# Kernel optimization log

Hardware: AMD Instinct MI355X
Metric: run time of the kernel (lower is better)

Reference implementation:

```python
import jax, jax.numpy as jnp
import numpy as np

TAU_M = 5.0 / 3.0
V_TH = 1.0


def setup_inputs() -> dict:
    key = jax.random.key(0)
    T, B, C, H, W = 8, 32, 128, 32, 32
    x = jax.random.normal(key, (T, B, C, H, W), dtype=jnp.float32)
    return {"x": x}


def reference(x):
    """LIF neuron: leaky integrate, bidirectional threshold fire (+1/-1), hard reset.
    x: [T, B, C, H, W]. Returns spike train output: [T, B, C, H, W]."""
    def step(V, x_t):
        dv = -V / TAU_M + x_t          # leak + input current
        V_new = V + dv                  # integrate
        out = (V_new >= V_TH).astype(x_t.dtype) - (V_new <= -V_TH).astype(x_t.dtype)
        V_next = (1.0 - jnp.abs(out)) * V_new   # reset to 0 where spiked
        return V_next, out

    V0 = jnp.zeros_like(x[0])
    _, output = jax.lax.scan(step, V0, x)
    return output
```

## Files before the change

kernel.cpp:

```cpp
#include <hip/hip_runtime.h>


#define T_STEPS 8

typedef float vfloat4 __attribute__((ext_vector_type(4)));

struct StepOut { float V; float o; };

__device__ __forceinline__ StepOut lif_step(float V, float x) {
    const float TAU = (float)(5.0 / 3.0);
    float dv = (-V) / TAU + x;
    float Vn = V + dv;
    float o = (Vn >= 1.0f ? 1.0f : 0.0f) - (Vn <= -1.0f ? 1.0f : 0.0f);
    StepOut r;
    r.o = o;
    r.V = (o == 0.0f) ? Vn : 0.0f;
    return r;
}

__device__ __forceinline__ vfloat4 lif_step4(vfloat4& V, vfloat4 xt) {
    StepOut a = lif_step(V.x, xt.x);
    StepOut b = lif_step(V.y, xt.y);
    StepOut c = lif_step(V.z, xt.z);
    StepOut d = lif_step(V.w, xt.w);
    vfloat4 Vn, o;
    Vn.x = a.V; Vn.y = b.V; Vn.z = c.V; Vn.w = d.V;
    o.x = a.o;  o.y = b.o;  o.z = c.o;  o.w = d.o;
    V = Vn;
    return o;
}

__global__ __launch_bounds__(256) void lif_kernel(const vfloat4* __restrict__ x,
                                                  vfloat4* __restrict__ out,
                                                  int n4) {
    const int Q = n4 >> 2;
    int q = blockIdx.x * blockDim.x + threadIdx.x;
    if (q >= Q) return;

    const size_t s = (size_t)n4;
    const size_t i0 = (size_t)q;
    const size_t i1 = (size_t)q + (size_t)Q;
    const size_t i2 = (size_t)q + 2 * (size_t)Q;
    const size_t i3 = (size_t)q + 3 * (size_t)Q;

    vfloat4 Va = (vfloat4)(0.f);
    vfloat4 Vb = Va, Vc = Va, Vd = Va;

#pragma unroll
    for (int t = 0; t < T_STEPS; ++t) {
        const size_t base = (size_t)t * s;
        vfloat4 xa = x[base + i0];
        vfloat4 xb = x[base + i1];
        vfloat4 xc = x[base + i2];
        vfloat4 xd = x[base + i3];

        vfloat4 oa = lif_step4(Va, xa);
        vfloat4 ob = lif_step4(Vb, xb);
        vfloat4 oc = lif_step4(Vc, xc);
        vfloat4 od = lif_step4(Vd, xd);

        __builtin_nontemporal_store(oa, &out[base + i0]);
        __builtin_nontemporal_store(ob, &out[base + i1]);
        __builtin_nontemporal_store(oc, &out[base + i2]);
        __builtin_nontemporal_store(od, &out[base + i3]);
    }
}

extern "C" void kernel_launch(void* const* d_in, const int* in_sizes, int n_in,
                              void* d_out, int out_size, void* d_ws, size_t ws_size,
                              hipStream_t stream) {
    const float* x = (const float*)d_in[0];
    float* out = (float*)d_out;

    int total = in_sizes[0];
    int n = total / T_STEPS;
    int n4 = n / 4;
    int Q = n4 / 4;

    dim3 block(256);
    dim3 grid((Q + block.x - 1) / block.x);
    lif_kernel<<<grid, block, 0, stream>>>((const vfloat4*)x, (vfloat4*)out, n4);
}
```

Baseline: 232.0 us.

## Issue all timestep loads up front via inline asm, one vec4 per thread

Each thread now handles a single float4 column instead of four. All eight timestep loads are issued back to back through inline-asm global_load_dwordx4, followed by one explicit vmcnt(0) wait, so that every read is in flight before any compute starts. The grid grows 4x to keep enough parallelism, and stores switch from nontemporal to ordinary stores. The risks are that the hand-written asm and explicit wait limit the compiler's own scheduling, and that dropping nontemporal stores may pollute the cache.

```diff
diff --git a/kernel.cpp b/kernel.cpp
--- a/kernel.cpp
+++ b/kernel.cpp
@@ -30,40 +30,44 @@
     return o;
 }
 
-__global__ __launch_bounds__(256) void lif_kernel(const vfloat4* __restrict__ x,
-                                                  vfloat4* __restrict__ out,
+#define ASM_LOAD(dst, addr)                                        \
+    asm volatile("global_load_dwordx4 %0, %1, off"                 \
+                 : "=&v"(dst)                                      \
+                 : "v"(addr))
+
+__global__ __launch_bounds__(256) void lif_kernel(const float* __restrict__ x,
+                                                  float* __restrict__ out,
                                                   int n4) {
-    const int Q = n4 >> 2;
-    int q = blockIdx.x * blockDim.x + threadIdx.x;
-    if (q >= Q) return;
+    int i = blockIdx.x * blockDim.x + threadIdx.x;
+    if (i >= n4) return;
+
+    const unsigned long long stride = (unsigned long long)n4 * 16ull;
+    unsigned long long a = (unsigned long long)x + (unsigned long long)i * 16ull;
+
+    vfloat4 x0, x1, x2, x3, x4, x5, x6, x7;
+    ASM_LOAD(x0, a + 0 * stride);
+    ASM_LOAD(x1, a + 1 * stride);
+    ASM_LOAD(x2, a + 2 * stride);
+    ASM_LOAD(x3, a + 3 * stride);
+    ASM_LOAD(x4, a + 4 * stride);
+    ASM_LOAD(x5, a + 5 * stride);
+    ASM_LOAD(x6, a + 6 * stride);
+    ASM_LOAD(x7, a + 7 * stride);
+    asm volatile("s_waitcnt vmcnt(0)"
+                 : "+v"(x0), "+v"(x1), "+v"(x2), "+v"(x3),
+                   "+v"(x4), "+v"(x5), "+v"(x6), "+v"(x7));
 
     const size_t s = (size_t)n4;
-    const size_t i0 = (size_t)q;
-    const size_t i1 = (size_t)q + (size_t)Q;
-    const size_t i2 = (size_t)q + 2 * (size_t)Q;
-    const size_t i3 = (size_t)q + 3 * (size_t)Q;
-
-    vfloat4 Va = (vfloat4)(0.f);
-    vfloat4 Vb = Va, Vc = Va, Vd = Va;
-
-#pragma unroll
-    for (int t = 0; t < T_STEPS; ++t) {
-        const size_t base = (size_t)t * s;
-        vfloat4 xa = x[base + i0];
-        vfloat4 xb = x[base + i1];
-        vfloat4 xc = x[base + i2];
-        vfloat4 xd = x[base + i3];
-
-        vfloat4 oa = lif_step4(Va, xa);
-        vfloat4 ob = lif_step4(Vb, xb);
-        vfloat4 oc = lif_step4(Vc, xc);
-        vfloat4 od = lif_step4(Vd, xd);
-
-        __builtin_nontemporal_store(oa, &out[base + i0]);
-        __builtin_nontemporal_store(ob, &out[base + i1]);
-        __builtin_nontemporal_store(oc, &out[base + i2]);
-        __builtin_nontemporal_store(od, &out[base + i3]);
-    }
+    vfloat4* o4 = (vfloat4*)out;
+    vfloat4 V = (vfloat4)(0.f);
+    o4[0 * s + i] = lif_step4(V, x0);
+    o4[1 * s + i] = lif_step4(V, x1);
+    o4[2 * s + i] = lif_step4(V, x2);
+    o4[3 * s + i] = lif_step4(V, x3);
+    o4[4 * s + i] = lif_step4(V, x4);
+    o4[5 * s + i] = lif_step4(V, x5);
+    o4[6 * s + i] = lif_step4(V, x6);
+    o4[7 * s + i] = lif_step4(V, x7);
 }
 
 extern "C" void kernel_launch(void* const* d_in, const int* in_sizes, int n_in,
@@ -75,9 +79,8 @@
     int total = in_sizes[0];
     int n = total / T_STEPS;
     int n4 = n / 4;
-    int Q = n4 / 4;
 
     dim3 block(256);
-    dim3 grid((Q + block.x - 1) / block.x);
-    lif_kernel<<<grid, block, 0, stream>>>((const vfloat4*)x, (vfloat4*)out, n4);
+    dim3 grid((n4 + block.x - 1) / block.x);
+    lif_kernel<<<grid, block, 0, stream>>>(x, out, n4);
 }
```

Result: slower. 239.6 us (+3.2%).

## Split LIF into pack kernel with 2-bit spike codes and unpack kernel

Applied to the files above, without the earlier changes.

Splits the fused LIF kernel into two launches. The first loads all 8 timesteps at once with inline-asm loads and a single wait, computes the spikes and packs them as 2-bit codes into a 64-bit workspace word per float4 lane. The second reads those words and writes the decoded float outputs. The intent is to separate the read-heavy and write-heavy phases so each streams more efficiently, at the cost of an extra launch and a small workspace round trip.

```diff
diff --git a/kernel.cpp b/kernel.cpp
--- a/kernel.cpp
+++ b/kernel.cpp
@@ -18,6 +18,77 @@
     return r;
 }
 
+__device__ __forceinline__ unsigned enc(float o) {
+    return (o == 1.0f) ? 1u : ((o == -1.0f) ? 2u : 0u);
+}
+
+__device__ __forceinline__ float dec(unsigned c) {
+    return (c == 1u) ? 1.0f : ((c == 2u) ? -1.0f : 0.0f);
+}
+
+#define ASM_LOAD(dst, addr)                                        \
+    asm volatile("global_load_dwordx4 %0, %1, off"                 \
+                 : "=&v"(dst)                                      \
+                 : "v"(addr))
+
+__global__ __launch_bounds__(256) void lif_pack(const float* __restrict__ x,
+                                                unsigned long long* __restrict__ ws,
+                                                int n4) {
+    int i = blockIdx.x * blockDim.x + threadIdx.x;
+    if (i >= n4) return;
+
+    const unsigned long long stride = (unsigned long long)n4 * 16ull;
+    unsigned long long a = (unsigned long long)x + (unsigned long long)i * 16ull;
+
+    vfloat4 x0, x1, x2, x3, x4, x5, x6, x7;
+    ASM_LOAD(x0, a + 0 * stride);
+    ASM_LOAD(x1, a + 1 * stride);
+    ASM_LOAD(x2, a + 2 * stride);
+    ASM_LOAD(x3, a + 3 * stride);
+    ASM_LOAD(x4, a + 4 * stride);
+    ASM_LOAD(x5, a + 5 * stride);
+    ASM_LOAD(x6, a + 6 * stride);
+    ASM_LOAD(x7, a + 7 * stride);
+    asm volatile("s_waitcnt vmcnt(0)"
+                 : "+v"(x0), "+v"(x1), "+v"(x2), "+v"(x3),
+                   "+v"(x4), "+v"(x5), "+v"(x6), "+v"(x7));
+
+    vfloat4 xs[T_STEPS] = {x0, x1, x2, x3, x4, x5, x6, x7};
+    vfloat4 V = (vfloat4)(0.f);
+    unsigned long long acc = 0ull;
+#pragma unroll
+    for (int t = 0; t < T_STEPS; ++t) {
+        StepOut sa = lif_step(V.x, xs[t].x);
+        StepOut sb = lif_step(V.y, xs[t].y);
+        StepOut sc = lif_step(V.z, xs[t].z);
+        StepOut sd = lif_step(V.w, xs[t].w);
+        V.x = sa.V; V.y = sb.V; V.z = sc.V; V.w = sd.V;
+        unsigned byte = enc(sa.o) | (enc(sb.o) << 2) | (enc(sc.o) << 4) | (enc(sd.o) << 6);
+        acc |= ((unsigned long long)byte) << (8 * t);
+    }
+    ws[i] = acc;
+}
+
+__global__ __launch_bounds__(256) void lif_unpack(const unsigned long long* __restrict__ ws,
+                                                  vfloat4* __restrict__ out,
+                                                  int n4) {
+    int i = blockIdx.x * blockDim.x + threadIdx.x;
+    if (i >= n4) return;
+
+    unsigned long long u = ws[i];
+    const size_t s = (size_t)n4;
+#pragma unroll
+    for (int t = 0; t < T_STEPS; ++t) {
+        unsigned byte = (unsigned)(u >> (8 * t)) & 0xFFu;
+        vfloat4 o;
+        o.x = dec(byte & 3u);
+        o.y = dec((byte >> 2) & 3u);
+        o.z = dec((byte >> 4) & 3u);
+        o.w = dec((byte >> 6) & 3u);
+        __builtin_nontemporal_store(o, &out[(size_t)t * s + i]);
+    }
+}
+
 __device__ __forceinline__ vfloat4 lif_step4(vfloat4& V, vfloat4 xt) {
     StepOut a = lif_step(V.x, xt.x);
     StepOut b = lif_step(V.y, xt.y);
@@ -30,22 +101,19 @@
     return o;
 }
 
-__global__ __launch_bounds__(256) void lif_kernel(const vfloat4* __restrict__ x,
+__global__ __launch_bounds__(256) void lif_single(const vfloat4* __restrict__ x,
                                                   vfloat4* __restrict__ out,
                                                   int n4) {
     const int Q = n4 >> 2;
     int q = blockIdx.x * blockDim.x + threadIdx.x;
     if (q >= Q) return;
-
     const size_t s = (size_t)n4;
     const size_t i0 = (size_t)q;
     const size_t i1 = (size_t)q + (size_t)Q;
     const size_t i2 = (size_t)q + 2 * (size_t)Q;
     const size_t i3 = (size_t)q + 3 * (size_t)Q;
-
     vfloat4 Va = (vfloat4)(0.f);
     vfloat4 Vb = Va, Vc = Va, Vd = Va;
-
 #pragma unroll
     for (int t = 0; t < T_STEPS; ++t) {
         const size_t base = (size_t)t * s;
@@ -53,12 +121,10 @@
         vfloat4 xb = x[base + i1];
         vfloat4 xc = x[base + i2];
         vfloat4 xd = x[base + i3];
-
         vfloat4 oa = lif_step4(Va, xa);
         vfloat4 ob = lif_step4(Vb, xb);
         vfloat4 oc = lif_step4(Vc, xc);
         vfloat4 od = lif_step4(Vd, xd);
-
         __builtin_nontemporal_store(oa, &out[base + i0]);
         __builtin_nontemporal_store(ob, &out[base + i1]);
         __builtin_nontemporal_store(oc, &out[base + i2]);
@@ -75,9 +141,18 @@
     int total = in_sizes[0];
     int n = total / T_STEPS;
     int n4 = n / 4;
-    int Q = n4 / 4;
 
+    size_t need = (size_t)n4 * sizeof(unsigned long long);
     dim3 block(256);
-    dim3 grid((Q + block.x - 1) / block.x);
-    lif_kernel<<<grid, block, 0, stream>>>((const vfloat4*)x, (vfloat4*)out, n4);
+    dim3 grid((n4 + block.x - 1) / block.x);
+
+    if (ws_size >= need) {
+        unsigned long long* ws = (unsigned long long*)d_ws;
+        lif_pack<<<grid, block, 0, stream>>>(x, ws, n4);
+        lif_unpack<<<grid, block, 0, stream>>>(ws, (vfloat4*)out, n4);
+    } else {
+        int Q = n4 / 4;
+        dim3 grid1((Q + block.x - 1) / block.x);
+        lif_single<<<grid1, block, 0, stream>>>((const vfloat4*)x, (vfloat4*)out, n4);
+    }
 }
```

Measured after the change: 245.4 us. +5.8%, slower.
